# Performance work log

Measured on AMD Instinct MI355X. Metric: run time of the kernel, lower is better.

Reference implementation:

```python
import jax, jax.numpy as jnp
import numpy as np

ALPHA = 0.2          # LeakyReLU negative slope
NEG_INF = -9e15      # mask value from the original code


def setup_inputs() -> dict:
    key = jax.random.key(0)
    k1, k2, k3, k4 = jax.random.split(key, 4)
    B, N, F_in, F_out = 8, 2048, 64, 64
    x = jax.random.normal(k1, (B, N, F_in), dtype=jnp.float32)
    adj = jax.random.randint(k2, (B, N, N), 0, 2, dtype=jnp.int32)
    W = jax.random.normal(k3, (F_in, F_out), dtype=jnp.float32)
    a = jax.random.normal(k4, (2 * F_out, 1), dtype=jnp.float32)
    return {"x": x, "adj": adj, "W": W, "a": a}


def reference(x, adj, W, a):
    # h: [B, N, F_out]
    h = jnp.matmul(x, W)
    F_out = W.shape[1]
    a1 = a[:F_out, 0]   # source half of attention vector
    a2 = a[F_out:, 0]   # target half
    # e_ij = leakyrelu(h_i . a1 + h_j . a2)  -- identical math to the
    # original cat([h_i, h_j]) @ a without materializing [B,N*N,2F].
    s1 = jnp.einsum('bnf,f->bn', h, a1)  # [B, N]
    s2 = jnp.einsum('bnf,f->bn', h, a2)  # [B, N]
    e = jax.nn.leaky_relu(s1[:, :, None] + s2[:, None, :], negative_slope=ALPHA)
    masked = jnp.where(adj > 0, e, NEG_INF)
    attention = jax.nn.softmax(masked, axis=2)  # [B, N, N]
    # dropout p=0.0 / eval mode -> identity
    h_prime = jnp.matmul(attention, h)          # [B, N, F_out]
    return jax.nn.elu(h_prime)                  # concat=True branch
```

## Files before the change

### kernel.cpp

```cpp
#include <hip/hip_runtime.h>
#include <cstdint>

#define LRELU_ALPHA 0.2f
#define NEG_INF -9000000000000000.0f
#define L2E 1.4426950408889634f

typedef __bf16 bf16x8 __attribute__((ext_vector_type(8)));
typedef unsigned short ushortx8 __attribute__((ext_vector_type(8)));
typedef float floatx4 __attribute__((ext_vector_type(4)));

constexpr int Bb = 8, Nn = 2048, Ff = 64;
constexpr int TJ = 64;
constexpr int LSTR = 72;

__device__ __forceinline__ unsigned short f2bf(float f) {
    unsigned u = __builtin_bit_cast(unsigned, f);
    u = u + 0x7FFFu + ((u >> 16) & 1u);
    return (unsigned short)(u >> 16);
}

__global__ __launch_bounds__(256) void gat_prep(
    const float* __restrict__ x, const float* __restrict__ W, const float* __restrict__ a,
    unsigned short* __restrict__ hT, float* __restrict__ s1g, float* __restrict__ s2g)
{
    __shared__ unsigned short hblk[64 * LSTR];
    const int tid = threadIdx.x;
    const int blk = blockIdx.x;
    const int b  = blk >> 5;
    const int i0 = (blk & 31) * 64;
    const int w    = tid >> 6;
    const int lane = tid & 63;

    float wcol[64];
    #pragma unroll
    for (int k = 0; k < 64; ++k) wcol[k] = W[k * 64 + lane];
    const float a1 = a[lane], a2 = a[64 + lane];

    for (int r = 0; r < 16; ++r) {
        const int il = w * 16 + r;
        const int i  = i0 + il;
        const float* xrow = x + ((size_t)(b * Nn + i)) * 64;
        float h = 0.f;
        #pragma unroll
        for (int k = 0; k < 64; ++k) h = fmaf(xrow[k], wcol[k], h);
        float p1 = h * a1, p2 = h * a2;
        #pragma unroll
        for (int off = 32; off; off >>= 1) {
            p1 += __shfl_xor(p1, off);
            p2 += __shfl_xor(p2, off);
        }
        if (lane == 0) { s1g[b * Nn + i] = p1; s2g[b * Nn + i] = p2; }
        hblk[lane * LSTR + il] = f2bf(h);
    }
    __syncthreads();
    {
        const int f = tid >> 2, c = (tid & 3) * 16;
        const uint4* src = reinterpret_cast<const uint4*>(&hblk[f * LSTR + c]);
        uint4 v0 = src[0], v1 = src[1];
        uint4* dst = reinterpret_cast<uint4*>(hT + ((size_t)b * 64 + f) * Nn + i0 + c);
        dst[0] = v0; dst[1] = v1;
    }
}

__global__ __launch_bounds__(128) void gat_attn(
    const int* __restrict__ adj, const unsigned short* __restrict__ hT,
    const float* __restrict__ s1g, const float* __restrict__ s2g,
    float* __restrict__ out)
{
    __shared__ unsigned short hT_lds[64 * LSTR];
    __shared__ float s2_lds[TJ];

    const int tid  = threadIdx.x;
    const int blk  = blockIdx.x;
    const int gr0  = blk * 32;
    const int b    = gr0 >> 11;
    const int i0   = gr0 & 2047;
    const int w    = tid >> 6;
    const int lane = tid & 63;
    const int fl   = lane & 15;
    const int q    = lane >> 4;

    const int i = i0 + w * 16 + fl;
    const float s1v = s1g[b * Nn + i];
    const int* adj_row = adj + ((size_t)(b * Nn + i)) * Nn;
    const unsigned short* hTb = hT + (size_t)b * 64 * Nn;
    const float* s2b = s2g + b * Nn;

    float m = NEG_INF, l = 0.f;
    floatx4 C[4] = {};

    const int sf = tid >> 1, sc = (tid & 1) * 32;

    int4 adjv[4];
    {
        const int4* ap0 = reinterpret_cast<const int4*>(adj_row + q * 8);
        adjv[0] = ap0[0]; adjv[1] = ap0[1];
        const int4* ap1 = reinterpret_cast<const int4*>(adj_row + 32 + q * 8);
        adjv[2] = ap1[0]; adjv[3] = ap1[1];
    }

    for (int jt = 0; jt < Nn / TJ; ++jt) {
        const int j0 = jt * TJ;
        __syncthreads();
        {
            const uint4* gsrc = reinterpret_cast<const uint4*>(hTb + (size_t)sf * Nn + j0 + sc);
            uint4 g0 = gsrc[0], g1 = gsrc[1], g2 = gsrc[2], g3 = gsrc[3];
            uint4* ldst = reinterpret_cast<uint4*>(&hT_lds[sf * LSTR + sc]);
            ldst[0] = g0; ldst[1] = g1; ldst[2] = g2; ldst[3] = g3;
            if (tid < TJ) s2_lds[tid] = s2b[j0 + tid];
        }
        __syncthreads();

        int4 nadj[4] = {};
        if (jt + 1 < Nn / TJ) {
            const int* nrow = adj_row + j0 + TJ;
            const int4* ap0 = reinterpret_cast<const int4*>(nrow + q * 8);
            nadj[0] = ap0[0]; nadj[1] = ap0[1];
            const int4* ap1 = reinterpret_cast<const int4*>(nrow + 32 + q * 8);
            nadj[2] = ap1[0]; nadj[3] = ap1[1];
        }

        float e[16];
        const int* av = reinterpret_cast<const int*>(adjv);
        #pragma unroll
        for (int t = 0; t < 2; ++t) {
            float s2v[8];
            *reinterpret_cast<float4*>(&s2v[0]) =
                *reinterpret_cast<const float4*>(&s2_lds[t * 32 + q * 8]);
            *reinterpret_cast<float4*>(&s2v[4]) =
                *reinterpret_cast<const float4*>(&s2_lds[t * 32 + q * 8 + 4]);
            #pragma unroll
            for (int jj = 0; jj < 8; ++jj) {
                float ev = s1v + s2v[jj];
                ev = fmaxf(ev, LRELU_ALPHA * ev);
                e[t * 8 + jj] = (av[t * 8 + jj] > 0) ? ev : NEG_INF;
            }
        }
        float tmax = e[0];
        #pragma unroll
        for (int k = 1; k < 16; ++k) tmax = fmaxf(tmax, e[k]);
        tmax = fmaxf(tmax, __shfl_xor(tmax, 16));
        tmax = fmaxf(tmax, __shfl_xor(tmax, 32));
        const float m_new = fmaxf(m, tmax);
        const float alpha_s = exp2f((m - m_new) * L2E);
        m = m_new;

        float tsum = 0.f;
        unsigned short pb[16];
        #pragma unroll
        for (int k = 0; k < 16; ++k) {
            float p = exp2f((e[k] - m_new) * L2E);
            tsum += p;
            pb[k] = f2bf(p);
        }
        tsum += __shfl_xor(tsum, 16);
        tsum += __shfl_xor(tsum, 32);
        l = l * alpha_s + tsum;

        ushortx8 a0v, a1v;
        #pragma unroll
        for (int jj = 0; jj < 8; ++jj) { a0v[jj] = pb[jj]; a1v[jj] = pb[8 + jj]; }
        const bf16x8 A0 = __builtin_bit_cast(bf16x8, a0v);
        const bf16x8 A1 = __builtin_bit_cast(bf16x8, a1v);

        float ac[4];
        #pragma unroll
        for (int r = 0; r < 4; ++r) ac[r] = __shfl(alpha_s, q * 4 + r);
        #pragma unroll
        for (int u = 0; u < 4; ++u)
            #pragma unroll
            for (int r = 0; r < 4; ++r) C[u][r] *= ac[r];

        #pragma unroll
        for (int u = 0; u < 4; ++u) {
            const bf16x8 B0 = *reinterpret_cast<const bf16x8*>(
                &hT_lds[(u * 16 + fl) * LSTR + q * 8]);
            C[u] = __builtin_amdgcn_mfma_f32_16x16x32_bf16(A0, B0, C[u], 0, 0, 0);
            const bf16x8 B1 = *reinterpret_cast<const bf16x8*>(
                &hT_lds[(u * 16 + fl) * LSTR + 32 + q * 8]);
            C[u] = __builtin_amdgcn_mfma_f32_16x16x32_bf16(A1, B1, C[u], 0, 0, 0);
        }
        adjv[0] = nadj[0]; adjv[1] = nadj[1]; adjv[2] = nadj[2]; adjv[3] = nadj[3];
    }

    float lc[4];
    #pragma unroll
    for (int r = 0; r < 4; ++r) lc[r] = __shfl(l, q * 4 + r);
    #pragma unroll
    for (int u = 0; u < 4; ++u) {
        #pragma unroll
        for (int r = 0; r < 4; ++r) {
            float v = C[u][r] / lc[r];
            v = (v > 0.f) ? v : (exp2f(v * L2E) - 1.f);
            const int orow = i0 + w * 16 + q * 4 + r;
            out[((size_t)(b * Nn + orow)) * 64 + u * 16 + fl] = v;
        }
    }
}

extern "C" void kernel_launch(void* const* d_in, const int* in_sizes, int n_in,
                              void* d_out, int out_size, void* d_ws, size_t ws_size,
                              hipStream_t stream) {
    const float* x   = (const float*)d_in[0];
    const int*   adj = (const int*)d_in[1];
    const float* W   = (const float*)d_in[2];
    const float* a   = (const float*)d_in[3];
    float* out = (float*)d_out;

    unsigned short* hT = (unsigned short*)d_ws;
    float* s1 = (float*)((char*)d_ws + (size_t)Bb * 64 * Nn * sizeof(unsigned short));
    float* s2 = s1 + Bb * Nn;

    gat_prep<<<dim3(Bb * Nn / 64), dim3(256), 0, stream>>>(x, W, a, hT, s1, s2);
    gat_attn<<<dim3(Bb * Nn / 32), dim3(128), 0, stream>>>(adj, hT, s1, s2, out);
}
```

Before: 246.1 us.

## Split attention key dimension into segments with flash-decoding style merge kernel

```diff
diff --git a/kernel.cpp b/kernel.cpp
--- a/kernel.cpp
+++ b/kernel.cpp
@@ -12,6 +12,9 @@
 constexpr int Bb = 8, Nn = 2048, Ff = 64;
 constexpr int TJ = 64;
 constexpr int LSTR = 72;
+constexpr int SEG = 8;
+constexpr int SEGT = (Nn / TJ) / SEG;
+constexpr int NROWS = Bb * Nn;
 
 __device__ __forceinline__ unsigned short f2bf(float f) {
     unsigned u = __builtin_bit_cast(unsigned, f);
@@ -23,11 +26,12 @@
     const float* __restrict__ x, const float* __restrict__ W, const float* __restrict__ a,
     unsigned short* __restrict__ hT, float* __restrict__ s1g, float* __restrict__ s2g)
 {
-    __shared__ unsigned short hblk[64 * LSTR];
+    constexpr int STR2 = 36;
+    __shared__ unsigned short hblk[64 * STR2];
     const int tid = threadIdx.x;
     const int blk = blockIdx.x;
-    const int b  = blk >> 5;
-    const int i0 = (blk & 31) * 64;
+    const int b  = blk >> 6;
+    const int i0 = (blk & 63) * 32;
     const int w    = tid >> 6;
     const int lane = tid & 63;
 
@@ -36,8 +40,8 @@
     for (int k = 0; k < 64; ++k) wcol[k] = W[k * 64 + lane];
     const float a1 = a[lane], a2 = a[64 + lane];
 
-    for (int r = 0; r < 16; ++r) {
-        const int il = w * 16 + r;
+    for (int r = 0; r < 8; ++r) {
+        const int il = w * 8 + r;
         const int i  = i0 + il;
         const float* xrow = x + ((size_t)(b * Nn + i)) * 64;
         float h = 0.f;
@@ -50,29 +54,29 @@
             p2 += __shfl_xor(p2, off);
         }
         if (lane == 0) { s1g[b * Nn + i] = p1; s2g[b * Nn + i] = p2; }
-        hblk[lane * LSTR + il] = f2bf(h);
+        hblk[lane * STR2 + il] = f2bf(h);
     }
     __syncthreads();
     {
-        const int f = tid >> 2, c = (tid & 3) * 16;
-        const uint4* src = reinterpret_cast<const uint4*>(&hblk[f * LSTR + c]);
-        uint4 v0 = src[0], v1 = src[1];
-        uint4* dst = reinterpret_cast<uint4*>(hT + ((size_t)b * 64 + f) * Nn + i0 + c);
-        dst[0] = v0; dst[1] = v1;
+        const int f = tid >> 2, c = (tid & 3) * 8;
+        uint4 v = *reinterpret_cast<const uint4*>(&hblk[f * STR2 + c]);
+        *reinterpret_cast<uint4*>(hT + ((size_t)b * 64 + f) * Nn + i0 + c) = v;
     }
 }
 
 __global__ __launch_bounds__(128) void gat_attn(
     const int* __restrict__ adj, const unsigned short* __restrict__ hT,
     const float* __restrict__ s1g, const float* __restrict__ s2g,
-    float* __restrict__ out)
+    float* __restrict__ m_part, float* __restrict__ l_part, float* __restrict__ O_part)
 {
     __shared__ unsigned short hT_lds[64 * LSTR];
     __shared__ float s2_lds[TJ];
 
     const int tid  = threadIdx.x;
     const int blk  = blockIdx.x;
-    const int gr0  = blk * 32;
+    const int seg  = blk >> 9;
+    const int grp  = blk & 511;
+    const int gr0  = grp * 32;
     const int b    = gr0 >> 11;
     const int i0   = gr0 & 2047;
     const int w    = tid >> 6;
@@ -91,15 +95,18 @@
 
     const int sf = tid >> 1, sc = (tid & 1) * 32;
 
+    const int jt0 = seg * SEGT;
+
     int4 adjv[4];
     {
-        const int4* ap0 = reinterpret_cast<const int4*>(adj_row + q * 8);
+        const int* arow = adj_row + jt0 * TJ;
+        const int4* ap0 = reinterpret_cast<const int4*>(arow + q * 8);
         adjv[0] = ap0[0]; adjv[1] = ap0[1];
-        const int4* ap1 = reinterpret_cast<const int4*>(adj_row + 32 + q * 8);
+        const int4* ap1 = reinterpret_cast<const int4*>(arow + 32 + q * 8);
         adjv[2] = ap1[0]; adjv[3] = ap1[1];
     }
 
-    for (int jt = 0; jt < Nn / TJ; ++jt) {
+    for (int jt = jt0; jt < jt0 + SEGT; ++jt) {
         const int j0 = jt * TJ;
         __syncthreads();
         {
@@ -112,7 +119,7 @@
         __syncthreads();
 
         int4 nadj[4] = {};
-        if (jt + 1 < Nn / TJ) {
+        if (jt + 1 < jt0 + SEGT) {
             const int* nrow = adj_row + j0 + TJ;
             const int4* ap0 = reinterpret_cast<const int4*>(nrow + q * 8);
             nadj[0] = ap0[0]; nadj[1] = ap0[1];
@@ -146,20 +153,28 @@
         m = m_new;
 
         float tsum = 0.f;
-        unsigned short pb[16];
+        float p[16];
         #pragma unroll
         for (int k = 0; k < 16; ++k) {
-            float p = exp2f((e[k] - m_new) * L2E);
-            tsum += p;
-            pb[k] = f2bf(p);
+            p[k] = exp2f((e[k] - m_new) * L2E);
+            tsum += p[k];
         }
         tsum += __shfl_xor(tsum, 16);
         tsum += __shfl_xor(tsum, 32);
         l = l * alpha_s + tsum;
 
         ushortx8 a0v, a1v;
-        #pragma unroll
-        for (int jj = 0; jj < 8; ++jj) { a0v[jj] = pb[jj]; a1v[jj] = pb[8 + jj]; }
+#if __has_builtin(__builtin_amdgcn_cvt_pk_bf16_f32)
+        #pragma unroll
+        for (int jj = 0; jj < 4; ++jj) {
+            ushortx8* dst = jj < 2 ? &a0v : &a1v;
+        }
+        #pragma unroll
+        for (int jj = 0; jj < 8; ++jj) { a0v[jj] = f2bf(p[jj]); a1v[jj] = f2bf(p[8 + jj]); }
+#else
+        #pragma unroll
+        for (int jj = 0; jj < 8; ++jj) { a0v[jj] = f2bf(p[jj]); a1v[jj] = f2bf(p[8 + jj]); }
+#endif
         const bf16x8 A0 = __builtin_bit_cast(bf16x8, a0v);
         const bf16x8 A1 = __builtin_bit_cast(bf16x8, a1v);
 
@@ -183,19 +198,46 @@
         adjv[0] = nadj[0]; adjv[1] = nadj[1]; adjv[2] = nadj[2]; adjv[3] = nadj[3];
     }
 
-    float lc[4];
-    #pragma unroll
-    for (int r = 0; r < 4; ++r) lc[r] = __shfl(l, q * 4 + r);
+    if (q == 0) {
+        const int ri = b * Nn + i;
+        m_part[seg * NROWS + ri] = m;
+        l_part[seg * NROWS + ri] = l;
+    }
     #pragma unroll
     for (int u = 0; u < 4; ++u) {
         #pragma unroll
         for (int r = 0; r < 4; ++r) {
-            float v = C[u][r] / lc[r];
-            v = (v > 0.f) ? v : (exp2f(v * L2E) - 1.f);
             const int orow = i0 + w * 16 + q * 4 + r;
-            out[((size_t)(b * Nn + orow)) * 64 + u * 16 + fl] = v;
-        }
-    }
+            O_part[((size_t)seg * NROWS + b * Nn + orow) * 64 + u * 16 + fl] = C[u][r];
+        }
+    }
+}
+
+__global__ __launch_bounds__(256) void gat_merge(
+    const float* __restrict__ m_part, const float* __restrict__ l_part,
+    const float* __restrict__ O_part, float* __restrict__ out)
+{
+    const int tid = threadIdx.x;
+    const int ri  = blockIdx.x * 4 + (tid >> 6);
+    const int f   = tid & 63;
+
+    float mv[SEG];
+    #pragma unroll
+    for (int s = 0; s < SEG; ++s) mv[s] = m_part[s * NROWS + ri];
+    float mstar = mv[0];
+    #pragma unroll
+    for (int s = 1; s < SEG; ++s) mstar = fmaxf(mstar, mv[s]);
+
+    float lsum = 0.f, acc = 0.f;
+    #pragma unroll
+    for (int s = 0; s < SEG; ++s) {
+        const float wgt = exp2f((mv[s] - mstar) * L2E);
+        lsum += l_part[s * NROWS + ri] * wgt;
+        acc  += O_part[((size_t)s * NROWS + ri) * 64 + f] * wgt;
+    }
+    float v = acc / lsum;
+    v = (v > 0.f) ? v : (exp2f(v * L2E) - 1.f);
+    out[(size_t)ri * 64 + f] = v;
 }
 
 extern "C" void kernel_launch(void* const* d_in, const int* in_sizes, int n_in,
@@ -207,10 +249,16 @@
     const float* a   = (const float*)d_in[3];
     float* out = (float*)d_out;
 
-    unsigned short* hT = (unsigned short*)d_ws;
-    float* s1 = (float*)((char*)d_ws + (size_t)Bb * 64 * Nn * sizeof(unsigned short));
-    float* s2 = s1 + Bb * Nn;
-
-    gat_prep<<<dim3(Bb * Nn / 64), dim3(256), 0, stream>>>(x, W, a, hT, s1, s2);
-    gat_attn<<<dim3(Bb * Nn / 32), dim3(128), 0, stream>>>(adj, hT, s1, s2, out);
-}
+    char* p = (char*)d_ws;
+    unsigned short* hT = (unsigned short*)p;  p += (size_t)Bb * 64 * Nn * sizeof(unsigned short);
+    float* s1 = (float*)p;                    p += (size_t)NROWS * sizeof(float);
+    float* s2 = (float*)p;                    p += (size_t)NROWS * sizeof(float);
+    float* m_part = (float*)p;                p += (size_t)SEG * NROWS * sizeof(float);
+    float* l_part = (float*)p;                p += (size_t)SEG * NROWS * sizeof(float);
+    float* O_part = (float*)p;
+
+    gat_prep<<<dim3(Bb * Nn / 32), dim3(256), 0, stream>>>(x, W, a, hT, s1, s2);
+    gat_attn<<<dim3(SEG * (Bb * Nn / 32)), dim3(128), 0, stream>>>(
+        adj, hT, s1, s2, m_part, l_part, O_part);
+    gat_merge<<<dim3(NROWS / 4), dim3(256), 0, stream>>>(m_part, l_part, O_part, out);
+}
```

After: 237.9 us. 1.03x faster.
